# Kernel tuning notes

Hardware: AMD Instinct MI355X
Metric: run time of the kernel (lower is better)

The kernel has to match this reference:

```python
import jax, jax.numpy as jnp
import numpy as np
import random

EPS = 1e-16  # matches EKM eps default
B, M, N, R = 8, 8192, 512, 256


def setup_inputs() -> dict:
    key = jax.random.key(0)
    kx, = jax.random.split(key, 1)
    x = jax.random.normal(kx, (B, M, N), dtype=jnp.float32)
    # EKM init: random.seed(42); inds = random.sample(range(M), R)
    random.seed(42)
    inds = jnp.asarray(random.sample(range(M), R), dtype=jnp.int32)
    # EKMInit overrides ekm.alpha with nn.Parameter(torch.tensor([0.1]))
    alpha = jnp.asarray([0.1], dtype=jnp.float32)
    return {"x": x, "alpha": alpha, "inds": inds}


def _memberships(x, v, alpha):
    x2 = jnp.sum(x * x, axis=2, keepdims=True)           # (B, M, 1)
    xv = jnp.einsum('bmn,bnr->bmr', x, v)                # (B, M, R)
    v2 = jnp.sum(v * v, axis=1, keepdims=True)           # (B, 1, R)
    d = jax.nn.relu(x2 - 2.0 * xv + v2)
    return jax.nn.softmax(-d / alpha, axis=2)            # (B, M, R)


def reference(x, alpha, inds):
    # init: v0 = t(x[:, inds, :]) -> (B, N, R); u0 = memberships(x, v0)
    v0 = jnp.swapaxes(x[:, inds, :], 1, 2)               # (B, N, R)
    # solver step (num_iters=1): u_new = memberships(x, v0) (== u0),
    # v_new = centers(x, u_new)
    u = _memberships(x, v0, alpha)                       # (B, M, R)
    u_n = (u + EPS) / (jnp.sum(u, axis=1, keepdims=True) + EPS)
    v = jnp.einsum('bmn,bmr->bnr', x, u_n)               # (B, N, R)
    return (u, v)
```

## Files before the change

kernel.cpp:

```cpp
#include <hip/hip_runtime.h>
#include <math.h>

#define B 8
#define M 8192
#define N 512
#define R 256
#define EPSF 1e-16f

typedef __attribute__((ext_vector_type(8))) short short8;
typedef __attribute__((ext_vector_type(16))) float f32x16;

__device__ __forceinline__ unsigned short bf16_rtn(float f) {
    unsigned int u = __float_as_uint(f);
    u += 0x7FFFu + ((u >> 16) & 1u);
    return (unsigned short)(u >> 16);
}

__device__ __forceinline__ void gll16(const unsigned short* g, unsigned short* l) {
    __builtin_amdgcn_global_load_lds(
        (const __attribute__((address_space(1))) unsigned int*)g,
        (__attribute__((address_space(3))) unsigned int*)l, 16, 0, 0);
}

__global__ __launch_bounds__(256) void ekm_kc(
    const float* __restrict__ x, const int* __restrict__ inds,
    unsigned short* __restrict__ c_hi, unsigned short* __restrict__ c_lo,
    float* __restrict__ v2g)
{
    const int t = threadIdx.x, b = blockIdx.y;
    const int r = blockIdx.x * 16 + (t >> 4);
    const int seg = (t & 15) * 32;
    const float* src = x + ((size_t)b * M + inds[r]) * N + seg;
    unsigned short* hd = c_hi + ((size_t)b * R + r) * 512 + seg;
    unsigned short* ld = c_lo + ((size_t)b * R + r) * 512 + seg;
    float vp = 0.f;
#pragma unroll
    for (int c = 0; c < 4; ++c) {
        float4 f0 = *(const float4*)(src + c * 8);
        float4 f1 = *(const float4*)(src + c * 8 + 4);
        float av[8] = {f0.x, f0.y, f0.z, f0.w, f1.x, f1.y, f1.z, f1.w};
        unsigned ph[4], pl[4];
#pragma unroll
        for (int j = 0; j < 4; ++j) {
            vp += av[2*j] * av[2*j] + av[2*j+1] * av[2*j+1];
            unsigned short h0 = bf16_rtn(av[2*j]), h1 = bf16_rtn(av[2*j+1]);
            float r0 = av[2*j]   - __uint_as_float((unsigned)h0 << 16);
            float r1 = av[2*j+1] - __uint_as_float((unsigned)h1 << 16);
            ph[j] = (unsigned)h0 | ((unsigned)h1 << 16);
            pl[j] = (unsigned)bf16_rtn(r0) | ((unsigned)bf16_rtn(r1) << 16);
        }
        *(uint4*)(hd + c * 8) = make_uint4(ph[0], ph[1], ph[2], ph[3]);
        *(uint4*)(ld + c * 8) = make_uint4(pl[0], pl[1], pl[2], pl[3]);
    }
    vp += __shfl_xor(vp, 1); vp += __shfl_xor(vp, 2);
    vp += __shfl_xor(vp, 4); vp += __shfl_xor(vp, 8);
    if ((t & 15) == 0) v2g[b * R + r] = vp;
}

__global__ __launch_bounds__(256, 2) void ekm_k1(
    const float* __restrict__ x, const float* __restrict__ alpha_p,
    const unsigned short* __restrict__ c_hi, const unsigned short* __restrict__ c_lo,
    const float* __restrict__ v2g, float* __restrict__ u_out,
    unsigned short* __restrict__ uT, unsigned short* __restrict__ xT,
    float* __restrict__ colsum)
{
    __shared__ unsigned short Bh[2][8192], Bl[2][8192];
    __shared__ unsigned short Ah[2][2048], Al[2][2048];

    const int t = threadIdx.x;
    const int b = blockIdx.y;
    const int m0 = blockIdx.x * 64;
    const int w = t >> 6, l = t & 63, col = l & 31, h5 = l >> 5;
    const int arow = t >> 2, kch = t & 3;
    const int cswz = (t & 3) ^ ((t >> 3) & 3);
    const int pswz = (col >> 1) & 3;
    const int aws = arow * 32 + (kch ^ ((arow >> 1) & 3)) * 8;

    const float* ax = x + ((size_t)b * M + m0 + arow) * N + kch * 8;
    const unsigned short* bhs = c_hi + ((size_t)b * R + (t >> 2)) * 512 + cswz * 8;
    const unsigned short* bls = c_lo + ((size_t)b * R + (t >> 2)) * 512 + cswz * 8;

    f32x16 acc[2][2];
    acc[0][0] = (f32x16)0.f; acc[0][1] = (f32x16)0.f;
    acc[1][0] = (f32x16)0.f; acc[1][1] = (f32x16)0.f;

    float x2p = 0.f;
    unsigned ph[4], pl[4];
    float4 a0, a1;

    auto convert = [&](void) {
        float av[8] = {a0.x, a0.y, a0.z, a0.w, a1.x, a1.y, a1.z, a1.w};
#pragma unroll
        for (int j = 0; j < 4; ++j) {
            x2p += av[2*j] * av[2*j] + av[2*j+1] * av[2*j+1];
            unsigned short h0 = bf16_rtn(av[2*j]), h1 = bf16_rtn(av[2*j+1]);
            float r0 = av[2*j]   - __uint_as_float((unsigned)h0 << 16);
            float r1 = av[2*j+1] - __uint_as_float((unsigned)h1 << 16);
            ph[j] = (unsigned)h0 | ((unsigned)h1 << 16);
            pl[j] = (unsigned)bf16_rtn(r0) | ((unsigned)bf16_rtn(r1) << 16);
        }
    };

    auto mfma_tile = [&](int c) {
#pragma unroll
        for (int half = 0; half < 2; ++half) {
            const int pc = (half * 2 + h5) ^ pswz;
            short8 ahf[2], alf[2], bhf[2], blf[2];
#pragma unroll
            for (int tm = 0; tm < 2; ++tm) {
                ahf[tm] = *(const short8*)&Ah[c][(tm*32 + col) * 32 + pc * 8];
                alf[tm] = *(const short8*)&Al[c][(tm*32 + col) * 32 + pc * 8];
            }
#pragma unroll
            for (int tr = 0; tr < 2; ++tr) {
                bhf[tr] = *(const short8*)&Bh[c][(w*64 + tr*32 + col) * 32 + pc * 8];
                blf[tr] = *(const short8*)&Bl[c][(w*64 + tr*32 + col) * 32 + pc * 8];
            }
#pragma unroll
            for (int tm = 0; tm < 2; ++tm)
#pragma unroll
            for (int tr = 0; tr < 2; ++tr) {
                acc[tm][tr] = __builtin_amdgcn_mfma_f32_32x32x16_bf16(ahf[tm], bhf[tr], acc[tm][tr], 0, 0, 0);
                acc[tm][tr] = __builtin_amdgcn_mfma_f32_32x32x16_bf16(ahf[tm], blf[tr], acc[tm][tr], 0, 0, 0);
                acc[tm][tr] = __builtin_amdgcn_mfma_f32_32x32x16_bf16(alf[tm], bhf[tr], acc[tm][tr], 0, 0, 0);
            }
        }
    };

    auto xt_store = [&](int c, int tt) {
        int kk = t >> 3, ms = (t & 7) * 8;
        unsigned short vv[8];
#pragma unroll
        for (int i = 0; i < 8; ++i) {
            int row = ms + i;
            vv[i] = Ah[c][row * 32 + (((kk >> 3) ^ ((row >> 1) & 3)) << 3) + (kk & 7)];
        }
        *(uint4*)(xT + ((size_t)b * N + tt * 32 + kk) * M + m0 + ms) =
            make_uint4((unsigned)vv[0] | ((unsigned)vv[1] << 16),
                       (unsigned)vv[2] | ((unsigned)vv[3] << 16),
                       (unsigned)vv[4] | ((unsigned)vv[5] << 16),
                       (unsigned)vv[6] | ((unsigned)vv[7] << 16));
    };

    a0 = *(const float4*)(ax);
    a1 = *(const float4*)(ax + 4);
    convert();
#pragma unroll
    for (int i = 0; i < 4; ++i) {
        gll16(bhs + i * (64 * 512), &Bh[0][i * 2048 + t * 8]);
        gll16(bls + i * (64 * 512), &Bl[0][i * 2048 + t * 8]);
    }
    __builtin_amdgcn_sched_barrier(0);
    *(uint4*)&Ah[0][aws] = make_uint4(ph[0], ph[1], ph[2], ph[3]);
    *(uint4*)&Al[0][aws] = make_uint4(pl[0], pl[1], pl[2], pl[3]);
    a0 = *(const float4*)(ax + 32);
    a1 = *(const float4*)(ax + 36);
    asm volatile("s_waitcnt vmcnt(2) lgkmcnt(0)" ::: "memory");
    __builtin_amdgcn_s_barrier();
    __builtin_amdgcn_sched_barrier(0);

    auto body = [&](int tt, int c, int nb) {
        convert();
#pragma unroll
        for (int i = 0; i < 4; ++i) {
            gll16(bhs + (tt + 1) * 32 + i * (64 * 512), &Bh[nb][i * 2048 + t * 8]);
            gll16(bls + (tt + 1) * 32 + i * (64 * 512), &Bl[nb][i * 2048 + t * 8]);
        }
        __builtin_amdgcn_sched_barrier(0);
        *(uint4*)&Ah[nb][aws] = make_uint4(ph[0], ph[1], ph[2], ph[3]);
        *(uint4*)&Al[nb][aws] = make_uint4(pl[0], pl[1], pl[2], pl[3]);
        const int pf = (tt + 2 < 16 ? tt + 2 : 15) * 32;
        a0 = *(const float4*)(ax + pf);
        a1 = *(const float4*)(ax + pf + 4);
        xt_store(c, tt);
        mfma_tile(c);
        asm volatile("s_waitcnt vmcnt(3) lgkmcnt(0)" ::: "memory");
        __builtin_amdgcn_s_barrier();
        __builtin_amdgcn_sched_barrier(0);
    };

#pragma unroll 1
    for (int tp = 0; tp < 7; ++tp) {
        body(2 * tp, 0, 1);
        body(2 * tp + 1, 1, 0);
    }
    body(14, 0, 1);
    mfma_tile(1);
    xt_store(1, 15);

    float* x2s = (float*)&Al[0][0];
    float (*redm)[64] = (float (*)[64])&Bh[0][0];
    float (*reds)[64] = (float (*)[64])&Bh[0][2048];

    x2p += __shfl_xor(x2p, 1);
    x2p += __shfl_xor(x2p, 2);
    if (kch == 0) x2s[arow] = x2p;
    __syncthreads();

    const float ia = 1.4426950408889634f / alpha_p[0];
    float v2c[2];
#pragma unroll
    for (int tr = 0; tr < 2; ++tr)
        v2c[tr] = v2g[b * R + w * 64 + tr * 32 + col];

#pragma unroll
    for (int tm = 0; tm < 2; ++tm)
#pragma unroll
    for (int reg = 0; reg < 16; ++reg) {
        int rowl = (reg & 3) + 8 * (reg >> 2) + 4 * h5;
        float x2v = x2s[tm * 32 + rowl];
        float mn;
#pragma unroll
        for (int tr = 0; tr < 2; ++tr) {
            float d = x2v - 2.f * acc[tm][tr][reg] + v2c[tr];
            d = fmaxf(d, 0.f);
            acc[tm][tr][reg] = d;
            mn = (tr == 0) ? d : fminf(mn, d);
        }
        mn = fminf(mn, __shfl_xor(mn, 1));
        mn = fminf(mn, __shfl_xor(mn, 2));
        mn = fminf(mn, __shfl_xor(mn, 4));
        mn = fminf(mn, __shfl_xor(mn, 8));
        mn = fminf(mn, __shfl_xor(mn, 16));
        if (col == 0) redm[w][tm * 32 + rowl] = mn;
    }
    __syncthreads();

#pragma unroll
    for (int tm = 0; tm < 2; ++tm)
#pragma unroll
    for (int reg = 0; reg < 16; ++reg) {
        int m = tm * 32 + (reg & 3) + 8 * (reg >> 2) + 4 * h5;
        float mn = fminf(fminf(redm[0][m], redm[1][m]), fminf(redm[2][m], redm[3][m]));
        float s = 0.f;
#pragma unroll
        for (int tr = 0; tr < 2; ++tr) {
            float e = exp2f((mn - acc[tm][tr][reg]) * ia);
            acc[tm][tr][reg] = e;
            s += e;
        }
        s += __shfl_xor(s, 1); s += __shfl_xor(s, 2); s += __shfl_xor(s, 4);
        s += __shfl_xor(s, 8); s += __shfl_xor(s, 16);
        if (col == 0) reds[w][m] = s;
    }
    __syncthreads();

    float* ub = u_out + ((size_t)b * M + m0) * R + w * 64;
    float cs[2] = {0.f, 0.f};
#pragma unroll
    for (int tm = 0; tm < 2; ++tm)
#pragma unroll
    for (int reg = 0; reg < 16; ++reg) {
        int rowl = (reg & 3) + 8 * (reg >> 2) + 4 * h5;
        int m = tm * 32 + rowl;
        float inv = 1.f / (reds[0][m] + reds[1][m] + reds[2][m] + reds[3][m]);
#pragma unroll
        for (int tr = 0; tr < 2; ++tr) {
            float uu = acc[tm][tr][reg] * inv;
            acc[tm][tr][reg] = uu;
            ub[(size_t)m * R + tr * 32 + col] = uu;
            cs[tr] += uu;
        }
    }
    unsigned short* uTb = uT + ((size_t)b * R + w * 64) * M + m0;
#pragma unroll
    for (int tm = 0; tm < 2; ++tm)
#pragma unroll
    for (int tr = 0; tr < 2; ++tr)
#pragma unroll
    for (int rq = 0; rq < 4; ++rq) {
        uint2 p;
        p.x = (unsigned)bf16_rtn(acc[tm][tr][rq*4+0]) | ((unsigned)bf16_rtn(acc[tm][tr][rq*4+1]) << 16);
        p.y = (unsigned)bf16_rtn(acc[tm][tr][rq*4+2]) | ((unsigned)bf16_rtn(acc[tm][tr][rq*4+3]) << 16);
        *(uint2*)(uTb + (size_t)(tr*32 + col) * M + tm*32 + 8*rq + 4*h5) = p;
    }
    cs[0] += __shfl_xor(cs[0], 32);
    cs[1] += __shfl_xor(cs[1], 32);
    if (h5 == 0) {
        atomicAdd(&colsum[b * R + w * 64 + col], cs[0]);
        atomicAdd(&colsum[b * R + w * 64 + 32 + col], cs[1]);
    }
}

__global__ __launch_bounds__(256, 2) void ekm_k2(
    const unsigned short* __restrict__ xT, const unsigned short* __restrict__ uT,
    float* __restrict__ part)
{
    __shared__ unsigned short XA[2][8192], UB[2][8192];
    const int t = threadIdx.x;
    const int nt = blockIdx.x >> 1, rt = blockIdx.x & 1;
    const int slab = blockIdx.y, b = blockIdx.z;
    const int n0 = nt * 128, r0 = rt * 128;
    const int w = t >> 6, l = t & 63, col = l & 31, h5 = l >> 5;
    const int wn = w >> 1, wr = w & 1;
    const int srow = t >> 3;
    const int chunk = (t & 7) ^ (srow & 7);
    const int rx = col & 7;

    const unsigned short* xs = xT + ((size_t)b * N + n0 + srow) * M + (size_t)slab * 1024 + chunk * 8;
    const unsigned short* us = uT + ((size_t)b * R + r0 + srow) * M + (size_t)slab * 1024 + chunk * 8;

    f32x16 acc[2][2];
    acc[0][0] = (f32x16)0.f; acc[0][1] = (f32x16)0.f;
    acc[1][0] = (f32x16)0.f; acc[1][1] = (f32x16)0.f;

#pragma unroll
    for (int i = 0; i < 4; ++i) {
        gll16(xs + (size_t)i * 32 * M, &XA[0][i * 2048 + t * 8]);
        gll16(us + (size_t)i * 32 * M, &UB[0][i * 2048 + t * 8]);
    }
    asm volatile("s_waitcnt vmcnt(0)" ::: "memory");
    __builtin_amdgcn_s_barrier();
    __builtin_amdgcn_sched_barrier(0);

    auto body = [&](int tt, int c, int nb, bool stage) {
        if (stage) {
#pragma unroll
            for (int i = 0; i < 4; ++i) {
                gll16(xs + (tt + 1) * 64 + (size_t)i * 32 * M, &XA[nb][i * 2048 + t * 8]);
                gll16(us + (tt + 1) * 64 + (size_t)i * 32 * M, &UB[nb][i * 2048 + t * 8]);
            }
            __builtin_amdgcn_sched_barrier(0);
        }
#pragma unroll
        for (int kk = 0; kk < 4; ++kk) {
            const int pc = (kk * 2 + h5) ^ rx;
            short8 af[2], bf2[2];
#pragma unroll
            for (int tm = 0; tm < 2; ++tm)
                af[tm] = *(const short8*)&XA[c][(wn*64 + tm*32 + col) * 64 + pc * 8];
#pragma unroll
            for (int tr = 0; tr < 2; ++tr)
                bf2[tr] = *(const short8*)&UB[c][(wr*64 + tr*32 + col) * 64 + pc * 8];
#pragma unroll
            for (int tm = 0; tm < 2; ++tm)
#pragma unroll
            for (int tr = 0; tr < 2; ++tr)
                acc[tm][tr] = __builtin_amdgcn_mfma_f32_32x32x16_bf16(af[tm], bf2[tr], acc[tm][tr], 0, 0, 0);
        }
        if (stage) {
            asm volatile("s_waitcnt vmcnt(0)" ::: "memory");
            __builtin_amdgcn_s_barrier();
            __builtin_amdgcn_sched_barrier(0);
        }
    };

#pragma unroll 1
    for (int tp = 0; tp < 7; ++tp) {
        body(2 * tp, 0, 1, true);
        body(2 * tp + 1, 1, 0, true);
    }
    body(14, 0, 1, true);
    body(15, 1, 0, false);

    float* pb = part + (size_t)slab * ((size_t)B * N * R) + (size_t)b * N * R;
#pragma unroll
    for (int tm = 0; tm < 2; ++tm)
#pragma unroll
    for (int reg = 0; reg < 16; ++reg) {
        int n = n0 + wn*64 + tm*32 + (reg & 3) + 8*(reg >> 2) + 4*h5;
#pragma unroll
        for (int tr = 0; tr < 2; ++tr)
            pb[(size_t)n * R + r0 + wr*64 + tr*32 + col] = acc[tm][tr][reg];
    }
}

__global__ __launch_bounds__(256) void ekm_red(
    const float* __restrict__ part, const float* __restrict__ colsum,
    float* __restrict__ v_out)
{
    size_t o = ((size_t)blockIdx.x * 256 + threadIdx.x) * 4;
    float sx = 0.f, sy = 0.f, sz = 0.f, sw = 0.f;
#pragma unroll
    for (int sl = 0; sl < 8; ++sl) {
        float4 p = *(const float4*)(part + (size_t)sl * B * N * R + o);
        sx += p.x; sy += p.y; sz += p.z; sw += p.w;
    }
    int b = (int)(o >> 17);
    int r = (int)(o & (R - 1));
    float4 cs = *(const float4*)(colsum + b * R + r);
    float4 vo;
    vo.x = sx / (cs.x + EPSF);
    vo.y = sy / (cs.y + EPSF);
    vo.z = sz / (cs.z + EPSF);
    vo.w = sw / (cs.w + EPSF);
    *(float4*)(v_out + o) = vo;
}

extern "C" void kernel_launch(void* const* d_in, const int* in_sizes, int n_in,
                              void* d_out, int out_size, void* d_ws, size_t ws_size,
                              hipStream_t stream) {
    const float* x     = (const float*)d_in[0];
    const float* alpha = (const float*)d_in[1];
    const int*   inds  = (const int*)d_in[2];

    float* u_out = (float*)d_out;
    float* v_out = u_out + (size_t)B * M * R;

    char* ws = (char*)d_ws;
    const size_t CH = (size_t)B * R * 512 * 2;
    unsigned short* c_hi   = (unsigned short*)ws;
    unsigned short* c_lo   = (unsigned short*)(ws + CH);
    float*          v2g    = (float*)(ws + 2 * CH);
    float*          colsum = (float*)(ws + 2 * CH + (size_t)B * R * 4);
    char* p = ws + 2 * CH + 2 * (size_t)B * R * 4;
    unsigned short* xT = (unsigned short*)p;          p += (size_t)B * N * M * 2;
    unsigned short* uT = (unsigned short*)p;          p += (size_t)B * R * M * 2;
    float*          part = (float*)p;

    hipMemsetAsync(colsum, 0, (size_t)B * R * sizeof(float), stream);

    ekm_kc<<<dim3(16, B), 256, 0, stream>>>(x, inds, c_hi, c_lo, v2g);
    ekm_k1<<<dim3(M / 64, B), 256, 0, stream>>>(x, alpha, c_hi, c_lo, v2g,
                                                u_out, uT, xT, colsum);
    ekm_k2<<<dim3(8, 8, B), 256, 0, stream>>>(xT, uT, part);
    ekm_red<<<(B * N * R / 4) / 256, 256, 0, stream>>>(part, colsum, v_out);
}
```

Before: 348.2 us.

## Halve K-tile in distance GEMM, deepen k2 pipeline to four stages, remap blocks

The membership kernel now uses 16-wide K tiles with half the shared memory, so launch bounds allow 4 blocks per CU, and the grid is flattened with the batch index in the low bits. The center GEMM kernel switches to 32-wide K tiles with a 4-buffer pipeline holding three loads in flight, and an XCD-aware block index remap. The aim is more occupancy and better hiding of global-to-LDS latency, at the cost of more barriers per K and new swizzle patterns.

```diff
diff --git a/kernel.cpp b/kernel.cpp
--- a/kernel.cpp
+++ b/kernel.cpp
@@ -57,136 +57,127 @@
     if ((t & 15) == 0) v2g[b * R + r] = vp;
 }
 
-__global__ __launch_bounds__(256, 2) void ekm_k1(
+__global__ __launch_bounds__(256, 4) void ekm_k1(
     const float* __restrict__ x, const float* __restrict__ alpha_p,
     const unsigned short* __restrict__ c_hi, const unsigned short* __restrict__ c_lo,
     const float* __restrict__ v2g, float* __restrict__ u_out,
     unsigned short* __restrict__ uT, unsigned short* __restrict__ xT,
     float* __restrict__ colsum)
 {
-    __shared__ unsigned short Bh[2][8192], Bl[2][8192];
-    __shared__ unsigned short Ah[2][2048], Al[2][2048];
+    __shared__ unsigned short Bh[2][4096], Bl[2][4096];
+    __shared__ unsigned short Ah[2][1024], Al[2][1024];
 
     const int t = threadIdx.x;
-    const int b = blockIdx.y;
-    const int m0 = blockIdx.x * 64;
+    const int b = blockIdx.x & 7;
+    const int m0 = (blockIdx.x >> 3) * 64;
     const int w = t >> 6, l = t & 63, col = l & 31, h5 = l >> 5;
-    const int arow = t >> 2, kch = t & 3;
-    const int cswz = (t & 3) ^ ((t >> 3) & 3);
-    const int pswz = (col >> 1) & 3;
-    const int aws = arow * 32 + (kch ^ ((arow >> 1) & 3)) * 8;
-
-    const float* ax = x + ((size_t)b * M + m0 + arow) * N + kch * 8;
-    const unsigned short* bhs = c_hi + ((size_t)b * R + (t >> 2)) * 512 + cswz * 8;
-    const unsigned short* bls = c_lo + ((size_t)b * R + (t >> 2)) * 512 + cswz * 8;
+    const int arow = t >> 2, kq = t & 3;
+    const int swz1 = (col >> 2) & 1;
+    const int ari0 = ((col * 2 + h5) ^ swz1) * 8;
+    const int ari1 = ((64 + col * 2 + h5) ^ swz1) * 8;
+    const int bri0 = ((w * 128 + col * 2 + h5) ^ swz1) * 8;
+    const int bri1 = ((w * 128 + 64 + col * 2 + h5) ^ swz1) * 8;
+    const int awi = ((arow * 2 + (kq >> 1)) ^ ((arow >> 2) & 1)) * 8 + (kq & 1) * 4;
+
+    const float* ax = x + ((size_t)b * M + m0 + arow) * N + kq * 4;
+    const int bso = ((t & 1) ^ ((t >> 3) & 1)) * 8;
+    const unsigned short* bhs = c_hi + ((size_t)b * R + (t >> 1)) * 512 + bso;
+    const unsigned short* bls = c_lo + ((size_t)b * R + (t >> 1)) * 512 + bso;
 
     f32x16 acc[2][2];
     acc[0][0] = (f32x16)0.f; acc[0][1] = (f32x16)0.f;
     acc[1][0] = (f32x16)0.f; acc[1][1] = (f32x16)0.f;
 
     float x2p = 0.f;
-    unsigned ph[4], pl[4];
-    float4 a0, a1;
+    unsigned ph0, ph1, pl0, pl1;
+    float4 a0;
 
     auto convert = [&](void) {
-        float av[8] = {a0.x, a0.y, a0.z, a0.w, a1.x, a1.y, a1.z, a1.w};
-#pragma unroll
-        for (int j = 0; j < 4; ++j) {
+        float av[4] = {a0.x, a0.y, a0.z, a0.w};
+        unsigned hp[2], lp[2];
+#pragma unroll
+        for (int j = 0; j < 2; ++j) {
             x2p += av[2*j] * av[2*j] + av[2*j+1] * av[2*j+1];
             unsigned short h0 = bf16_rtn(av[2*j]), h1 = bf16_rtn(av[2*j+1]);
             float r0 = av[2*j]   - __uint_as_float((unsigned)h0 << 16);
             float r1 = av[2*j+1] - __uint_as_float((unsigned)h1 << 16);
-            ph[j] = (unsigned)h0 | ((unsigned)h1 << 16);
-            pl[j] = (unsigned)bf16_rtn(r0) | ((unsigned)bf16_rtn(r1) << 16);
-        }
+            hp[j] = (unsigned)h0 | ((unsigned)h1 << 16);
+            lp[j] = (unsigned)bf16_rtn(r0) | ((unsigned)bf16_rtn(r1) << 16);
+        }
+        ph0 = hp[0]; ph1 = hp[1]; pl0 = lp[0]; pl1 = lp[1];
     };
 
     auto mfma_tile = [&](int c) {
-#pragma unroll
-        for (int half = 0; half < 2; ++half) {
-            const int pc = (half * 2 + h5) ^ pswz;
-            short8 ahf[2], alf[2], bhf[2], blf[2];
-#pragma unroll
-            for (int tm = 0; tm < 2; ++tm) {
-                ahf[tm] = *(const short8*)&Ah[c][(tm*32 + col) * 32 + pc * 8];
-                alf[tm] = *(const short8*)&Al[c][(tm*32 + col) * 32 + pc * 8];
-            }
-#pragma unroll
-            for (int tr = 0; tr < 2; ++tr) {
-                bhf[tr] = *(const short8*)&Bh[c][(w*64 + tr*32 + col) * 32 + pc * 8];
-                blf[tr] = *(const short8*)&Bl[c][(w*64 + tr*32 + col) * 32 + pc * 8];
-            }
-#pragma unroll
-            for (int tm = 0; tm < 2; ++tm)
-#pragma unroll
-            for (int tr = 0; tr < 2; ++tr) {
-                acc[tm][tr] = __builtin_amdgcn_mfma_f32_32x32x16_bf16(ahf[tm], bhf[tr], acc[tm][tr], 0, 0, 0);
-                acc[tm][tr] = __builtin_amdgcn_mfma_f32_32x32x16_bf16(ahf[tm], blf[tr], acc[tm][tr], 0, 0, 0);
-                acc[tm][tr] = __builtin_amdgcn_mfma_f32_32x32x16_bf16(alf[tm], bhf[tr], acc[tm][tr], 0, 0, 0);
-            }
+        short8 bh0 = *(const short8*)&Bh[c][bri0];
+        short8 bl0 = *(const short8*)&Bl[c][bri0];
+        short8 bh1 = *(const short8*)&Bh[c][bri1];
+        short8 bl1 = *(const short8*)&Bl[c][bri1];
+#pragma unroll
+        for (int tm = 0; tm < 2; ++tm) {
+            short8 ah = *(const short8*)&Ah[c][tm ? ari1 : ari0];
+            short8 al = *(const short8*)&Al[c][tm ? ari1 : ari0];
+            acc[tm][0] = __builtin_amdgcn_mfma_f32_32x32x16_bf16(ah, bh0, acc[tm][0], 0, 0, 0);
+            acc[tm][0] = __builtin_amdgcn_mfma_f32_32x32x16_bf16(ah, bl0, acc[tm][0], 0, 0, 0);
+            acc[tm][0] = __builtin_amdgcn_mfma_f32_32x32x16_bf16(al, bh0, acc[tm][0], 0, 0, 0);
+            acc[tm][1] = __builtin_amdgcn_mfma_f32_32x32x16_bf16(ah, bh1, acc[tm][1], 0, 0, 0);
+            acc[tm][1] = __builtin_amdgcn_mfma_f32_32x32x16_bf16(ah, bl1, acc[tm][1], 0, 0, 0);
+            acc[tm][1] = __builtin_amdgcn_mfma_f32_32x32x16_bf16(al, bh1, acc[tm][1], 0, 0, 0);
         }
     };
 
     auto xt_store = [&](int c, int tt) {
-        int kk = t >> 3, ms = (t & 7) * 8;
-        unsigned short vv[8];
-#pragma unroll
-        for (int i = 0; i < 8; ++i) {
-            int row = ms + i;
-            vv[i] = Ah[c][row * 32 + (((kk >> 3) ^ ((row >> 1) & 3)) << 3) + (kk & 7)];
-        }
-        *(uint4*)(xT + ((size_t)b * N + tt * 32 + kk) * M + m0 + ms) =
-            make_uint4((unsigned)vv[0] | ((unsigned)vv[1] << 16),
-                       (unsigned)vv[2] | ((unsigned)vv[3] << 16),
-                       (unsigned)vv[4] | ((unsigned)vv[5] << 16),
-                       (unsigned)vv[6] | ((unsigned)vv[7] << 16));
+        int kk = t >> 4, ms = (t & 15) * 4;
+        unsigned short vv[4];
+#pragma unroll
+        for (int j = 0; j < 4; ++j) {
+            int row = ms + j;
+            vv[j] = Ah[c][((row * 2 + (kk >> 3)) ^ ((row >> 2) & 1)) * 8 + (kk & 7)];
+        }
+        *(uint2*)(xT + ((size_t)b * N + tt * 16 + kk) * M + m0 + ms) =
+            make_uint2((unsigned)vv[0] | ((unsigned)vv[1] << 16),
+                       (unsigned)vv[2] | ((unsigned)vv[3] << 16));
     };
 
     a0 = *(const float4*)(ax);
-    a1 = *(const float4*)(ax + 4);
     convert();
-#pragma unroll
-    for (int i = 0; i < 4; ++i) {
-        gll16(bhs + i * (64 * 512), &Bh[0][i * 2048 + t * 8]);
-        gll16(bls + i * (64 * 512), &Bl[0][i * 2048 + t * 8]);
-    }
-    __builtin_amdgcn_sched_barrier(0);
-    *(uint4*)&Ah[0][aws] = make_uint4(ph[0], ph[1], ph[2], ph[3]);
-    *(uint4*)&Al[0][aws] = make_uint4(pl[0], pl[1], pl[2], pl[3]);
-    a0 = *(const float4*)(ax + 32);
-    a1 = *(const float4*)(ax + 36);
-    asm volatile("s_waitcnt vmcnt(2) lgkmcnt(0)" ::: "memory");
+    gll16(bhs,              &Bh[0][t * 8]);
+    gll16(bhs + 128 * 512,  &Bh[0][2048 + t * 8]);
+    gll16(bls,              &Bl[0][t * 8]);
+    gll16(bls + 128 * 512,  &Bl[0][2048 + t * 8]);
+    __builtin_amdgcn_sched_barrier(0);
+    *(uint2*)&Ah[0][awi] = make_uint2(ph0, ph1);
+    *(uint2*)&Al[0][awi] = make_uint2(pl0, pl1);
+    a0 = *(const float4*)(ax + 16);
+    asm volatile("s_waitcnt vmcnt(1) lgkmcnt(0)" ::: "memory");
     __builtin_amdgcn_s_barrier();
     __builtin_amdgcn_sched_barrier(0);
 
     auto body = [&](int tt, int c, int nb) {
         convert();
-#pragma unroll
-        for (int i = 0; i < 4; ++i) {
-            gll16(bhs + (tt + 1) * 32 + i * (64 * 512), &Bh[nb][i * 2048 + t * 8]);
-            gll16(bls + (tt + 1) * 32 + i * (64 * 512), &Bl[nb][i * 2048 + t * 8]);
-        }
+        gll16(bhs + (tt + 1) * 16,             &Bh[nb][t * 8]);
+        gll16(bhs + 128 * 512 + (tt + 1) * 16, &Bh[nb][2048 + t * 8]);
+        gll16(bls + (tt + 1) * 16,             &Bl[nb][t * 8]);
+        gll16(bls + 128 * 512 + (tt + 1) * 16, &Bl[nb][2048 + t * 8]);
         __builtin_amdgcn_sched_barrier(0);
-        *(uint4*)&Ah[nb][aws] = make_uint4(ph[0], ph[1], ph[2], ph[3]);
-        *(uint4*)&Al[nb][aws] = make_uint4(pl[0], pl[1], pl[2], pl[3]);
-        const int pf = (tt + 2 < 16 ? tt + 2 : 15) * 32;
+        *(uint2*)&Ah[nb][awi] = make_uint2(ph0, ph1);
+        *(uint2*)&Al[nb][awi] = make_uint2(pl0, pl1);
+        const int pf = (tt + 2 < 32 ? tt + 2 : 31) * 16;
         a0 = *(const float4*)(ax + pf);
-        a1 = *(const float4*)(ax + pf + 4);
         xt_store(c, tt);
         mfma_tile(c);
-        asm volatile("s_waitcnt vmcnt(3) lgkmcnt(0)" ::: "memory");
+        asm volatile("s_waitcnt vmcnt(2) lgkmcnt(0)" ::: "memory");
         __builtin_amdgcn_s_barrier();
         __builtin_amdgcn_sched_barrier(0);
     };
 
 #pragma unroll 1
-    for (int tp = 0; tp < 7; ++tp) {
+    for (int tp = 0; tp < 15; ++tp) {
         body(2 * tp, 0, 1);
         body(2 * tp + 1, 1, 0);
     }
-    body(14, 0, 1);
+    body(30, 0, 1);
     mfma_tile(1);
-    xt_store(1, 15);
+    xt_store(1, 31);
 
     float* x2s = (float*)&Al[0][0];
     float (*redm)[64] = (float (*)[64])&Bh[0][0];
@@ -194,7 +185,7 @@
 
     x2p += __shfl_xor(x2p, 1);
     x2p += __shfl_xor(x2p, 2);
-    if (kch == 0) x2s[arow] = x2p;
+    if (kq == 0) x2s[arow] = x2p;
     __syncthreads();
 
     const float ia = 1.4426950408889634f / alpha_p[0];
@@ -286,72 +277,84 @@
     const unsigned short* __restrict__ xT, const unsigned short* __restrict__ uT,
     float* __restrict__ part)
 {
-    __shared__ unsigned short XA[2][8192], UB[2][8192];
+    __shared__ unsigned short XA[4][4096], UB[4][4096];
+
     const int t = threadIdx.x;
-    const int nt = blockIdx.x >> 1, rt = blockIdx.x & 1;
-    const int slab = blockIdx.y, b = blockIdx.z;
+    const int lin = blockIdx.x;
+    const int xcd = lin & 7, idx = lin >> 3;
+    const int ntrt = idx & 7, sb = (xcd << 3) | (idx >> 3);
+    const int slab = sb & 7, b = sb >> 3;
+    const int nt = ntrt >> 1, rt = ntrt & 1;
     const int n0 = nt * 128, r0 = rt * 128;
     const int w = t >> 6, l = t & 63, col = l & 31, h5 = l >> 5;
     const int wn = w >> 1, wr = w & 1;
-    const int srow = t >> 3;
-    const int chunk = (t & 7) ^ (srow & 7);
-    const int rx = col & 7;
-
-    const unsigned short* xs = xT + ((size_t)b * N + n0 + srow) * M + (size_t)slab * 1024 + chunk * 8;
-    const unsigned short* us = uT + ((size_t)b * R + r0 + srow) * M + (size_t)slab * 1024 + chunk * 8;
+    const int swz2 = (col >> 1) & 3;
+
+    const int srow = t >> 2;
+    const int ks = (t & 3) ^ ((t >> 3) & 3);
+    const unsigned short* xs = xT + ((size_t)b * N + n0 + srow) * M + (size_t)slab * 1024 + ks * 8;
+    const unsigned short* us = uT + ((size_t)b * R + r0 + srow) * M + (size_t)slab * 1024 + ks * 8;
 
     f32x16 acc[2][2];
     acc[0][0] = (f32x16)0.f; acc[0][1] = (f32x16)0.f;
     acc[1][0] = (f32x16)0.f; acc[1][1] = (f32x16)0.f;
 
-#pragma unroll
-    for (int i = 0; i < 4; ++i) {
-        gll16(xs + (size_t)i * 32 * M, &XA[0][i * 2048 + t * 8]);
-        gll16(us + (size_t)i * 32 * M, &UB[0][i * 2048 + t * 8]);
-    }
+    auto stageK = [&](int tt, unsigned short* xa, unsigned short* ub2) {
+        gll16(xs + tt * 32,                  xa + t * 8);
+        gll16(xs + tt * 32 + (size_t)64 * M, xa + 2048 + t * 8);
+        gll16(us + tt * 32,                  ub2 + t * 8);
+        gll16(us + tt * 32 + (size_t)64 * M, ub2 + 2048 + t * 8);
+    };
+    auto computeK = [&](const unsigned short* xa, const unsigned short* ub2) {
+#pragma unroll
+        for (int ch = 0; ch < 2; ++ch) {
+            const int pc = (ch * 2 + h5) ^ swz2;
+            short8 af0 = *(const short8*)&xa[(wn * 64 + col) * 32 + pc * 8];
+            short8 af1 = *(const short8*)&xa[(wn * 64 + 32 + col) * 32 + pc * 8];
+            short8 bf0 = *(const short8*)&ub2[(wr * 64 + col) * 32 + pc * 8];
+            short8 bf1 = *(const short8*)&ub2[(wr * 64 + 32 + col) * 32 + pc * 8];
+            acc[0][0] = __builtin_amdgcn_mfma_f32_32x32x16_bf16(af0, bf0, acc[0][0], 0, 0, 0);
+            acc[0][1] = __builtin_amdgcn_mfma_f32_32x32x16_bf16(af0, bf1, acc[0][1], 0, 0, 0);
+            acc[1][0] = __builtin_amdgcn_mfma_f32_32x32x16_bf16(af1, bf0, acc[1][0], 0, 0, 0);
+            acc[1][1] = __builtin_amdgcn_mfma_f32_32x32x16_bf16(af1, bf1, acc[1][1], 0, 0, 0);
+        }
+    };
+
+    stageK(0, &XA[0][0], &UB[0][0]);
+    stageK(1, &XA[1][0], &UB[1][0]);
+    stageK(2, &XA[2][0], &UB[2][0]);
+    asm volatile("s_waitcnt vmcnt(8)" ::: "memory");
+    __builtin_amdgcn_s_barrier();
+    __builtin_amdgcn_sched_barrier(0);
+
+#pragma unroll 1
+    for (int t4 = 0; t4 < 28; t4 += 4) {
+#pragma unroll
+        for (int j = 0; j < 4; ++j) {
+            const int cb = j & 3, nb = (j + 3) & 3;
+            stageK(t4 + j + 3, &XA[nb][0], &UB[nb][0]);
+            __builtin_amdgcn_sched_barrier(0);
+            computeK(&XA[cb][0], &UB[cb][0]);
+            asm volatile("s_waitcnt vmcnt(8)" ::: "memory");
+            __builtin_amdgcn_s_barrier();
+            __builtin_amdgcn_sched_barrier(0);
+        }
+    }
+    stageK(31, &XA[3][0], &UB[3][0]);
+    __builtin_amdgcn_sched_barrier(0);
+    computeK(&XA[0][0], &UB[0][0]);
+    asm volatile("s_waitcnt vmcnt(8)" ::: "memory");
+    __builtin_amdgcn_s_barrier();
+    __builtin_amdgcn_sched_barrier(0);
+    computeK(&XA[1][0], &UB[1][0]);
+    asm volatile("s_waitcnt vmcnt(4)" ::: "memory");
+    __builtin_amdgcn_s_barrier();
+    __builtin_amdgcn_sched_barrier(0);
+    computeK(&XA[2][0], &UB[2][0]);
     asm volatile("s_waitcnt vmcnt(0)" ::: "memory");
     __builtin_amdgcn_s_barrier();
     __builtin_amdgcn_sched_barrier(0);
-
-    auto body = [&](int tt, int c, int nb, bool stage) {
-        if (stage) {
-#pragma unroll
-            for (int i = 0; i < 4; ++i) {
-                gll16(xs + (tt + 1) * 64 + (size_t)i * 32 * M, &XA[nb][i * 2048 + t * 8]);
-                gll16(us + (tt + 1) * 64 + (size_t)i * 32 * M, &UB[nb][i * 2048 + t * 8]);
-            }
-            __builtin_amdgcn_sched_barrier(0);
-        }
-#pragma unroll
-        for (int kk = 0; kk < 4; ++kk) {
-            const int pc = (kk * 2 + h5) ^ rx;
-            short8 af[2], bf2[2];
-#pragma unroll
-            for (int tm = 0; tm < 2; ++tm)
-                af[tm] = *(const short8*)&XA[c][(wn*64 + tm*32 + col) * 64 + pc * 8];
-#pragma unroll
-            for (int tr = 0; tr < 2; ++tr)
-                bf2[tr] = *(const short8*)&UB[c][(wr*64 + tr*32 + col) * 64 + pc * 8];
-#pragma unroll
-            for (int tm = 0; tm < 2; ++tm)
-#pragma unroll
-            for (int tr = 0; tr < 2; ++tr)
-                acc[tm][tr] = __builtin_amdgcn_mfma_f32_32x32x16_bf16(af[tm], bf2[tr], acc[tm][tr], 0, 0, 0);
-        }
-        if (stage) {
-            asm volatile("s_waitcnt vmcnt(0)" ::: "memory");
-            __builtin_amdgcn_s_barrier();
-            __builtin_amdgcn_sched_barrier(0);
-        }
-    };
-
-#pragma unroll 1
-    for (int tp = 0; tp < 7; ++tp) {
-        body(2 * tp, 0, 1, true);
-        body(2 * tp + 1, 1, 0, true);
-    }
-    body(14, 0, 1, true);
-    body(15, 1, 0, false);
+    computeK(&XA[3][0], &UB[3][0]);
 
     float* pb = part + (size_t)slab * ((size_t)B * N * R) + (size_t)b * N * R;
 #pragma unroll
@@ -411,8 +414,8 @@
     hipMemsetAsync(colsum, 0, (size_t)B * R * sizeof(float), stream);
 
     ekm_kc<<<dim3(16, B), 256, 0, stream>>>(x, inds, c_hi, c_lo, v2g);
-    ekm_k1<<<dim3(M / 64, B), 256, 0, stream>>>(x, alpha, c_hi, c_lo, v2g,
-                                                u_out, uT, xT, colsum);
-    ekm_k2<<<dim3(8, 8, B), 256, 0, stream>>>(xT, uT, part);
+    ekm_k1<<<dim3(1024), 256, 0, stream>>>(x, alpha, c_hi, c_lo, v2g,
+                                           u_out, uT, xT, colsum);
+    ekm_k2<<<dim3(512), 256, 0, stream>>>(xT, uT, part);
     ekm_red<<<(B * N * R / 4) / 256, 256, 0, stream>>>(part, colsum, v_out);
 }
```

Result: slower. 391.4 us (+12.4%).
